# Kernel optimization log

Hardware: AMD Instinct MI355X
Metric: run time of the kernel (lower is better)

## Reference

```python
import jax, jax.numpy as jnp
import numpy as np

INPUTDIM = 512
OUTDIM = 512
GRIDSIZE = 50


def setup_inputs() -> dict:
    key = jax.random.key(0)
    k1, k2 = jax.random.split(key)
    x = jax.random.normal(k1, (8, 256, INPUTDIM), dtype=jnp.float32)
    scale = 1.0 / (np.sqrt(INPUTDIM) * np.sqrt(GRIDSIZE))
    fouriercoeffs = jax.random.normal(k2, (2 * GRIDSIZE, INPUTDIM, OUTDIM), dtype=jnp.float32) * scale
    bias = jnp.zeros((OUTDIM,), dtype=jnp.float32)
    return {"x": x, "fouriercoeffs": fouriercoeffs, "bias": bias}


def reference(x, fouriercoeffs, bias):
    # x: (B, W, I); fouriercoeffs: (2G, I, O); bias: (O,)
    B, W, I = x.shape
    G = fouriercoeffs.shape[0] // 2
    k = jnp.arange(1, G + 1, dtype=x.dtype)  # (G,)
    angles = x[..., None] * k * jnp.pi  # (B, W, I, G)
    # features: (B, W, I, 2G) with [sin | cos] order matching torch.cat
    features = jnp.concatenate([jnp.sin(angles), jnp.cos(angles)], axis=-1)
    features = features.reshape(B * W, I, 2 * G)
    y = jnp.einsum("bik,kio->bo", features, fouriercoeffs)  # (B*W, O)
    y = y.reshape(B, W, -1) + bias
    return y
```

## Files before the change

kernel.cpp:

```cpp
#include <hip/hip_runtime.h>
#include <hip/hip_bf16.h>

#define NS 100
#define TILE_BYTES 8192

typedef float f32x4 __attribute__((ext_vector_type(4)));
typedef short s16x8 __attribute__((ext_vector_type(8)));
typedef unsigned int u32x4 __attribute__((ext_vector_type(4)));

static __device__ __forceinline__ unsigned int bfpack(float a, float b) {
  unsigned int ua = __builtin_bit_cast(unsigned int, a);
  unsigned int ub = __builtin_bit_cast(unsigned int, b);
  return ((ua + 0x8000u) >> 16) | ((ub + 0x8000u) & 0xFFFF0000u);
}

__global__ void fkan_zero(float* __restrict__ out) {
  int idx = blockIdx.x * 256 + threadIdx.x;
  f32x4 z = {0.f, 0.f, 0.f, 0.f};
  *(f32x4*)(out + (size_t)idx * 4) = z;
}

__global__ void fkan_prep(const float* __restrict__ C, unsigned short* __restrict__ Bt) {
  __shared__ float ldsF[32][132];
  const int bx = blockIdx.x;
  const int s = bx % NS;
  const int spnt = bx / NS;
  const int sp = spnt & 15, nt = spnt >> 4;
  const int f = (s >> 1) + 50 * (s & 1);
  const int t = threadIdx.x;

  const float* src = C + ((size_t)f * 512 + sp * 32) * 512 + nt * 128;
  const int col4 = t & 31, row0 = t >> 5;
  #pragma unroll
  for (int rep = 0; rep < 4; ++rep) {
    int r = row0 + rep * 8;
    f32x4 v = *(const f32x4*)(src + (size_t)r * 512 + col4 * 4);
    *(f32x4*)&ldsF[r][col4 * 4] = v;
  }
  __syncthreads();

  char* dst = (char*)Bt + (size_t)(spnt * NS + s) * TILE_BYTES;
  const int o = t & 127;
  const int c0 = t >> 7;
  #pragma unroll
  for (int q = 0; q < 2; ++q) {
    int c = c0 + 2 * q;
    u32x4 p;
    p[0] = bfpack(ldsF[c*8+0][o], ldsF[c*8+1][o]);
    p[1] = bfpack(ldsF[c*8+2][o], ldsF[c*8+3][o]);
    p[2] = bfpack(ldsF[c*8+4][o], ldsF[c*8+5][o]);
    p[3] = bfpack(ldsF[c*8+6][o], ldsF[c*8+7][o]);
    *(u32x4*)(dst + o * 64 + ((c ^ ((o >> 1) & 3)) << 4)) = p;
  }
}

__global__ __launch_bounds__(256, 2) void fkan_gemm(
    const float* __restrict__ x, const unsigned short* __restrict__ Bt,
    const float* __restrict__ bias, float* __restrict__ out) {
  __shared__ __attribute__((aligned(16))) char Bs[2][TILE_BYTES];

  const int tid  = threadIdx.x;
  const int lane = tid & 63;
  const int wid  = tid >> 6;
  const int wm   = wid >> 1, wn = wid & 1;
  const int bid  = blockIdx.x;
  const int mt   = bid & 15;
  const int nt   = (bid >> 4) & 3;
  const int sp   = bid >> 6;
  const int m0 = mt * 128, n0 = nt * 128;
  const int lrow = lane & 15, lkg = lane >> 4;
  const int swz  = (lrow >> 1) & 3;

  float sk[4][8], ck[4][8], s1[4][8], c1[4][8];
  #pragma unroll
  for (int mi = 0; mi < 4; ++mi) {
    const float* xp = x + (size_t)(m0 + wm*64 + mi*16 + lrow) * 512 + sp*32 + lkg*8;
    f32x4 xa = *(const f32x4*)xp;
    f32x4 xb = *(const f32x4*)(xp + 4);
    #pragma unroll
    for (int j = 0; j < 8; ++j) {
      float xv = (j < 4) ? xa[j] : xb[j - 4];
      float r = xv * 0.5f;
      asm("v_fract_f32 %0, %1" : "=v"(r) : "v"(r));
      float sv, cv;
      asm("v_sin_f32 %0, %1" : "=v"(sv) : "v"(r));
      asm("v_cos_f32 %0, %1" : "=v"(cv) : "v"(r));
      s1[mi][j] = sv; c1[mi][j] = cv;
      sk[mi][j] = sv; ck[mi][j] = cv;
    }
  }

  f32x4 acc[4][4];
  #pragma unroll
  for (int mi = 0; mi < 4; ++mi)
    #pragma unroll
    for (int ni = 0; ni < 4; ++ni)
      acc[mi][ni] = (f32x4){0.f, 0.f, 0.f, 0.f};

  const char* gsrc = (const char*)Bt + (size_t)(nt * 16 + sp) * NS * TILE_BYTES + tid * 16;

  auto stage = [&](int buf) {
    __builtin_amdgcn_global_load_lds(
        (const __attribute__((address_space(1))) unsigned int*)(gsrc),
        (__attribute__((address_space(3))) unsigned int*)(&Bs[buf][tid * 16]), 16, 0, 0);
    __builtin_amdgcn_global_load_lds(
        (const __attribute__((address_space(1))) unsigned int*)(gsrc + 4096),
        (__attribute__((address_space(3))) unsigned int*)(&Bs[buf][4096 + tid * 16]), 16, 0, 0);
    gsrc += TILE_BYTES;
  };

  auto step = [&](int buf, float (&st)[4][8]) {
    s16x8 bfr[4];
    #pragma unroll
    for (int ni = 0; ni < 4; ++ni) {
      int o_loc = wn * 64 + ni * 16 + lrow;
      bfr[ni] = *(const s16x8*)(&Bs[buf][o_loc * 64 + ((lkg ^ swz) << 4)]);
    }
    #pragma unroll
    for (int mi = 0; mi < 4; ++mi) {
      u32x4 pk;
      pk[0] = bfpack(st[mi][0], st[mi][1]);
      pk[1] = bfpack(st[mi][2], st[mi][3]);
      pk[2] = bfpack(st[mi][4], st[mi][5]);
      pk[3] = bfpack(st[mi][6], st[mi][7]);
      s16x8 afr = __builtin_bit_cast(s16x8, pk);
      #pragma unroll
      for (int ni = 0; ni < 4; ++ni)
        acc[mi][ni] = __builtin_amdgcn_mfma_f32_16x16x32_bf16(afr, bfr[ni], acc[mi][ni], 0, 0, 0);
    }
  };

  stage(0);
  __syncthreads();
  int cur = 0;
  #pragma unroll 1
  for (int kh = 0; kh < 50; ++kh) {
    stage(cur ^ 1);
    step(cur, sk);
    __syncthreads();
    cur ^= 1;
    if (kh < 49) stage(cur ^ 1);
    step(cur, ck);
    #pragma unroll
    for (int mi = 0; mi < 4; ++mi)
      #pragma unroll
      for (int j = 0; j < 8; ++j) {
        float t1 = ck[mi][j] * s1[mi][j];
        float t2 = sk[mi][j] * s1[mi][j];
        sk[mi][j] = __builtin_fmaf(sk[mi][j], c1[mi][j], t1);
        ck[mi][j] = __builtin_fmaf(ck[mi][j], c1[mi][j], -t2);
      }
    __syncthreads();
    cur ^= 1;
  }

  #pragma unroll
  for (int ni = 0; ni < 4; ++ni) {
    const int col = n0 + wn * 64 + ni * 16 + lrow;
    const float bv = (sp == 0) ? bias[col] : 0.0f;
    #pragma unroll
    for (int mi = 0; mi < 4; ++mi) {
      const int row = m0 + wm * 64 + mi * 16 + lkg * 4;
      #pragma unroll
      for (int j = 0; j < 4; ++j)
        atomicAdd(out + (size_t)(row + j) * 512 + col, acc[mi][ni][j] + bv);
    }
  }
}

extern "C" void kernel_launch(void* const* d_in, const int* in_sizes, int n_in,
                              void* d_out, int out_size, void* d_ws, size_t ws_size,
                              hipStream_t stream) {
  const float* x    = (const float*)d_in[0];
  const float* C    = (const float*)d_in[1];
  const float* bias = (const float*)d_in[2];
  float* out = (float*)d_out;
  unsigned short* Bt = (unsigned short*)d_ws;

  fkan_zero<<<dim3(1024), dim3(256), 0, stream>>>(out);
  fkan_prep<<<dim3(6400), dim3(256), 0, stream>>>(C, Bt);
  fkan_gemm<<<dim3(1024), dim3(256), 0, stream>>>(x, Bt, bias, out);
}
```

Baseline: 346.2 us.

## Deepen LDS pipeline to four buffers with single barrier and packed math

The GEMM kernel moves from double buffering with two __syncthreads per half-step to a 4-slot LDS ring that prefetches two stages ahead, using a counted vmcnt wait and a single barrier per stage. It also raises MFMA priority with s_setprio and remaps block IDs so neighbouring blocks are spread across the grid. The software bf16 rounding is replaced with the hardware v_cvt_pk_bf16_f32 instruction, and the angle recurrence uses 2-wide float vectors to allow packed FMA. The prep kernel now writes output contiguously and applies the swizzle on the read side, and its LDS padding changes. The risks are higher LDS usage, which may limit occupancy, and a fragile hand-written waitcnt ordering.

```diff
diff --git a/kernel.cpp b/kernel.cpp
--- a/kernel.cpp
+++ b/kernel.cpp
@@ -5,13 +5,14 @@
 #define TILE_BYTES 8192
 
 typedef float f32x4 __attribute__((ext_vector_type(4)));
+typedef float f32x2 __attribute__((ext_vector_type(2)));
 typedef short s16x8 __attribute__((ext_vector_type(8)));
 typedef unsigned int u32x4 __attribute__((ext_vector_type(4)));
 
-static __device__ __forceinline__ unsigned int bfpack(float a, float b) {
-  unsigned int ua = __builtin_bit_cast(unsigned int, a);
-  unsigned int ub = __builtin_bit_cast(unsigned int, b);
-  return ((ua + 0x8000u) >> 16) | ((ub + 0x8000u) & 0xFFFF0000u);
+static __device__ __forceinline__ unsigned int cvtpk(float a, float b) {
+  unsigned int r;
+  asm("v_cvt_pk_bf16_f32 %0, %1, %2" : "=v"(r) : "v"(a), "v"(b));
+  return r;
 }
 
 __global__ void fkan_zero(float* __restrict__ out) {
@@ -21,7 +22,7 @@
 }
 
 __global__ void fkan_prep(const float* __restrict__ C, unsigned short* __restrict__ Bt) {
-  __shared__ float ldsF[32][132];
+  __shared__ float ldsF[32][136];
   const int bx = blockIdx.x;
   const int s = bx % NS;
   const int spnt = bx / NS;
@@ -40,30 +41,32 @@
   __syncthreads();
 
   char* dst = (char*)Bt + (size_t)(spnt * NS + s) * TILE_BYTES;
-  const int o = t & 127;
-  const int c0 = t >> 7;
   #pragma unroll
   for (int q = 0; q < 2; ++q) {
-    int c = c0 + 2 * q;
+    const int h = t + q * 256;
+    const int o = h >> 2;
+    const int ca = h & 3;
+    const int cd = ca ^ ((o >> 1) & 3);
     u32x4 p;
-    p[0] = bfpack(ldsF[c*8+0][o], ldsF[c*8+1][o]);
-    p[1] = bfpack(ldsF[c*8+2][o], ldsF[c*8+3][o]);
-    p[2] = bfpack(ldsF[c*8+4][o], ldsF[c*8+5][o]);
-    p[3] = bfpack(ldsF[c*8+6][o], ldsF[c*8+7][o]);
-    *(u32x4*)(dst + o * 64 + ((c ^ ((o >> 1) & 3)) << 4)) = p;
+    p[0] = cvtpk(ldsF[cd*8+0][o], ldsF[cd*8+1][o]);
+    p[1] = cvtpk(ldsF[cd*8+2][o], ldsF[cd*8+3][o]);
+    p[2] = cvtpk(ldsF[cd*8+4][o], ldsF[cd*8+5][o]);
+    p[3] = cvtpk(ldsF[cd*8+6][o], ldsF[cd*8+7][o]);
+    *(u32x4*)(dst + h * 16) = p;
   }
 }
 
 __global__ __launch_bounds__(256, 2) void fkan_gemm(
     const float* __restrict__ x, const unsigned short* __restrict__ Bt,
     const float* __restrict__ bias, float* __restrict__ out) {
-  __shared__ __attribute__((aligned(16))) char Bs[2][TILE_BYTES];
+  __shared__ __attribute__((aligned(16))) char Bs[4][TILE_BYTES];
 
   const int tid  = threadIdx.x;
   const int lane = tid & 63;
   const int wid  = tid >> 6;
   const int wm   = wid >> 1, wn = wid & 1;
-  const int bid  = blockIdx.x;
+  const int d    = blockIdx.x;
+  const int bid  = (d & 7) * 128 + (d >> 3);
   const int mt   = bid & 15;
   const int nt   = (bid >> 4) & 3;
   const int sp   = bid >> 6;
@@ -71,22 +74,26 @@
   const int lrow = lane & 15, lkg = lane >> 4;
   const int swz  = (lrow >> 1) & 3;
 
-  float sk[4][8], ck[4][8], s1[4][8], c1[4][8];
+  f32x2 sk[4][4], ck[4][4], s1[4][4], c1[4][4];
   #pragma unroll
   for (int mi = 0; mi < 4; ++mi) {
     const float* xp = x + (size_t)(m0 + wm*64 + mi*16 + lrow) * 512 + sp*32 + lkg*8;
     f32x4 xa = *(const f32x4*)xp;
     f32x4 xb = *(const f32x4*)(xp + 4);
     #pragma unroll
-    for (int j = 0; j < 8; ++j) {
-      float xv = (j < 4) ? xa[j] : xb[j - 4];
-      float r = xv * 0.5f;
-      asm("v_fract_f32 %0, %1" : "=v"(r) : "v"(r));
-      float sv, cv;
-      asm("v_sin_f32 %0, %1" : "=v"(sv) : "v"(r));
-      asm("v_cos_f32 %0, %1" : "=v"(cv) : "v"(r));
-      s1[mi][j] = sv; c1[mi][j] = cv;
-      sk[mi][j] = sv; ck[mi][j] = cv;
+    for (int p = 0; p < 4; ++p) {
+      #pragma unroll
+      for (int e = 0; e < 2; ++e) {
+        int j = p * 2 + e;
+        float xv = (j < 4) ? xa[j] : xb[j - 4];
+        float r = xv * 0.5f;
+        asm("v_fract_f32 %0, %1" : "=v"(r) : "v"(r));
+        float sv, cv;
+        asm("v_sin_f32 %0, %1" : "=v"(sv) : "v"(r));
+        asm("v_cos_f32 %0, %1" : "=v"(cv) : "v"(r));
+        s1[mi][p][e] = sv; c1[mi][p][e] = cv;
+        sk[mi][p][e] = sv; ck[mi][p][e] = cv;
+      }
     }
   }
 
@@ -99,59 +106,61 @@
 
   const char* gsrc = (const char*)Bt + (size_t)(nt * 16 + sp) * NS * TILE_BYTES + tid * 16;
 
-  auto stage = [&](int buf) {
+  auto stage = [&](int buf, int s) {
+    const char* p = gsrc + (size_t)s * TILE_BYTES;
     __builtin_amdgcn_global_load_lds(
-        (const __attribute__((address_space(1))) unsigned int*)(gsrc),
+        (const __attribute__((address_space(1))) unsigned int*)(p),
         (__attribute__((address_space(3))) unsigned int*)(&Bs[buf][tid * 16]), 16, 0, 0);
     __builtin_amdgcn_global_load_lds(
-        (const __attribute__((address_space(1))) unsigned int*)(gsrc + 4096),
+        (const __attribute__((address_space(1))) unsigned int*)(p + 4096),
         (__attribute__((address_space(3))) unsigned int*)(&Bs[buf][4096 + tid * 16]), 16, 0, 0);
-    gsrc += TILE_BYTES;
   };
 
-  auto step = [&](int buf, float (&st)[4][8]) {
+  auto iter = [&](int s, f32x2 (&st)[4][4]) {
+    s16x8 af[4];
+    #pragma unroll
+    for (int mi = 0; mi < 4; ++mi) {
+      u32x4 pk;
+      pk[0] = cvtpk(st[mi][0][0], st[mi][0][1]);
+      pk[1] = cvtpk(st[mi][1][0], st[mi][1][1]);
+      pk[2] = cvtpk(st[mi][2][0], st[mi][2][1]);
+      pk[3] = cvtpk(st[mi][3][0], st[mi][3][1]);
+      af[mi] = __builtin_bit_cast(s16x8, pk);
+    }
+    if (s < NS - 2) asm volatile("s_waitcnt vmcnt(2)" ::: "memory");
+    else            asm volatile("s_waitcnt vmcnt(0)" ::: "memory");
+    __builtin_amdgcn_s_barrier();
+    if (s < NS - 2) stage((s + 2) & 3, s + 2);
+    const char* base = &Bs[s & 3][0];
     s16x8 bfr[4];
     #pragma unroll
     for (int ni = 0; ni < 4; ++ni) {
       int o_loc = wn * 64 + ni * 16 + lrow;
-      bfr[ni] = *(const s16x8*)(&Bs[buf][o_loc * 64 + ((lkg ^ swz) << 4)]);
+      bfr[ni] = *(const s16x8*)(base + o_loc * 64 + ((lkg ^ swz) << 4));
     }
-    #pragma unroll
-    for (int mi = 0; mi < 4; ++mi) {
-      u32x4 pk;
-      pk[0] = bfpack(st[mi][0], st[mi][1]);
-      pk[1] = bfpack(st[mi][2], st[mi][3]);
-      pk[2] = bfpack(st[mi][4], st[mi][5]);
-      pk[3] = bfpack(st[mi][6], st[mi][7]);
-      s16x8 afr = __builtin_bit_cast(s16x8, pk);
-      #pragma unroll
-      for (int ni = 0; ni < 4; ++ni)
-        acc[mi][ni] = __builtin_amdgcn_mfma_f32_16x16x32_bf16(afr, bfr[ni], acc[mi][ni], 0, 0, 0);
-    }
-  };
-
-  stage(0);
-  __syncthreads();
-  int cur = 0;
-  #pragma unroll 1
-  for (int kh = 0; kh < 50; ++kh) {
-    stage(cur ^ 1);
-    step(cur, sk);
-    __syncthreads();
-    cur ^= 1;
-    if (kh < 49) stage(cur ^ 1);
-    step(cur, ck);
+    __builtin_amdgcn_s_setprio(1);
     #pragma unroll
     for (int mi = 0; mi < 4; ++mi)
       #pragma unroll
-      for (int j = 0; j < 8; ++j) {
-        float t1 = ck[mi][j] * s1[mi][j];
-        float t2 = sk[mi][j] * s1[mi][j];
-        sk[mi][j] = __builtin_fmaf(sk[mi][j], c1[mi][j], t1);
-        ck[mi][j] = __builtin_fmaf(ck[mi][j], c1[mi][j], -t2);
+      for (int ni = 0; ni < 4; ++ni)
+        acc[mi][ni] = __builtin_amdgcn_mfma_f32_16x16x32_bf16(af[mi], bfr[ni], acc[mi][ni], 0, 0, 0);
+    __builtin_amdgcn_s_setprio(0);
+  };
+
+  stage(0, 0);
+  stage(1, 1);
+  #pragma unroll 1
+  for (int kh = 0; kh < 50; ++kh) {
+    iter(2 * kh, sk);
+    iter(2 * kh + 1, ck);
+    #pragma unroll
+    for (int mi = 0; mi < 4; ++mi)
+      #pragma unroll
+      for (int p = 0; p < 4; ++p) {
+        f32x2 so = sk[mi][p], co = ck[mi][p];
+        sk[mi][p] = so * c1[mi][p] + co * s1[mi][p];
+        ck[mi][p] = co * c1[mi][p] - so * s1[mi][p];
       }
-    __syncthreads();
-    cur ^= 1;
   }
 
   #pragma unroll
```

Measured after the change: 314.6 us. -9.1%, faster.
